# Performance work log

Measured on AMD Instinct MI355X. Metric: run time of the kernel, lower is better.

The kernel has to match this reference:

```python
import jax, jax.numpy as jnp
import numpy as np

B, T, C, H = 2, 2048, 1024, 16
D = C // H  # head_dim = 64


def setup_inputs() -> dict:
    key = jax.random.key(0)
    k1, k2, k3, k4 = jax.random.split(key, 4)
    x = jax.random.normal(k1, (B, T, C), dtype=jnp.float32)
    # key_padding_mask: True for valid token, False for padding.
    # Use per-example valid lengths so the mask is realistic; every example
    # has length >= 1 so no softmax row is fully masked.
    lengths = jax.random.randint(k2, (B,), T // 2, T + 1)
    key_padding_mask = jnp.arange(T)[None, :] < lengths[:, None]
    Wqkv = jax.random.normal(k3, (3 * C, C), dtype=jnp.float32) * 0.02
    bqkv = jnp.zeros((3 * C,), dtype=jnp.float32)
    Wproj = jax.random.normal(k4, (C, C), dtype=jnp.float32) * 0.02
    bproj = jnp.zeros((C,), dtype=jnp.float32)
    return {"x": x, "key_padding_mask": key_padding_mask,
            "Wqkv": Wqkv, "bqkv": bqkv, "Wproj": Wproj, "bproj": bproj}


def reference(x, key_padding_mask, Wqkv, bqkv, Wproj, bproj):
    # qkv projection (torch Linear: y = x @ W^T + b)
    qkv = jnp.einsum('btc,oc->bto', x, Wqkv) + bqkv          # (B,T,3C)
    q, k, v = jnp.split(qkv, 3, axis=-1)
    q = q.reshape(B, T, H, D)
    k = k.reshape(B, T, H, D)
    v = v.reshape(B, T, H, D)
    scale = 1.0 / np.sqrt(D).astype(np.float32)
    scores = jnp.einsum('bqhd,bkhd->bhqk', q, k) * scale      # (B,H,T,T)
    causal = jnp.tril(jnp.ones((T, T), dtype=bool))           # (T,T)
    mask = causal[None, None, :, :] & key_padding_mask[:, None, None, :]
    scores = jnp.where(mask, scores, -jnp.inf)
    attn = jax.nn.softmax(scores, axis=-1)                    # dropout p=0.0
    out = jnp.einsum('bhqk,bkhd->bqhd', attn, v).reshape(B, T, C)
    out = jnp.einsum('btc,oc->bto', out, Wproj) + bproj
    return out
```

## Files before the change

### kernel.cpp

```cpp
#include <hip/hip_runtime.h>
#include <hip/hip_bf16.h>
#include <stdint.h>

#define B_ 2
#define T_ 2048
#define C_ 1024
#define H_ 16
#define D_ 64

typedef __attribute__((ext_vector_type(8))) short bf16x8;
typedef __attribute__((ext_vector_type(4))) float f32x4;

__device__ __forceinline__ unsigned short f2bf(float f) {
  union { float f; uint32_t u; } c; c.f = f;
  uint32_t r = c.u + 0x7FFFu + ((c.u >> 16) & 1u);
  return (unsigned short)(r >> 16);
}

__device__ __forceinline__ uint32_t pack_bf16x2(float lo, float hi) {
  uint32_t r;
  asm("v_cvt_pk_bf16_f32 %0, %1, %2" : "=v"(r) : "v"(lo), "v"(hi));
  return r;
}

__device__ __forceinline__ void gload_lds16(const unsigned short* g,
                                            unsigned short* l) {
  __builtin_amdgcn_global_load_lds(
      (const __attribute__((address_space(1))) void*)(g),
      (__attribute__((address_space(3))) void*)(l), 16, 0, 0);
}

#define N4_X 1048576
#define N4_WQ 786432
#define N4_WP 262144
__global__ void cvt_all(const float* __restrict__ x,
                        const float* __restrict__ wqkv,
                        const float* __restrict__ wproj,
                        unsigned short* __restrict__ xb,
                        unsigned short* __restrict__ wq,
                        unsigned short* __restrict__ wp) {
  int i = blockIdx.x * 256 + threadIdx.x;
  const float* s; unsigned short* d; int j;
  if (i < N4_X) { s = x; d = xb; j = i; }
  else if (i < N4_X + N4_WQ) { s = wqkv; d = wq; j = i - N4_X; }
  else { s = wproj; d = wp; j = i - (N4_X + N4_WQ); }
  float4 v = ((const float4*)s)[j];
  ushort4 o;
  o.x = f2bf(v.x); o.y = f2bf(v.y); o.z = f2bf(v.z); o.w = f2bf(v.w);
  ((ushort4*)d)[j] = o;
}

__global__ void compute_lengths(const unsigned int* __restrict__ mask,
                                int* __restrict__ lens) {
  int lane = threadIdx.x;
  unsigned int w0 = mask[0];
  for (int b = 0; b < B_; ++b) {
    int cnt = 0;
    if (w0 == 1u) {
      for (int t = lane; t < T_; t += 64) cnt += (mask[(size_t)b * T_ + t] != 0u);
    } else if (w0 == 0x3F800000u) {
      const float* mf = (const float*)mask;
      for (int t = lane; t < T_; t += 64) cnt += (mf[(size_t)b * T_ + t] != 0.f);
    } else {
      const unsigned char* mb = (const unsigned char*)mask;
      for (int t = lane; t < T_; t += 64) cnt += (mb[(size_t)b * T_ + t] != 0);
    }
    for (int off = 32; off > 0; off >>= 1) cnt += __shfl_down(cnt, off);
    if (lane == 0) lens[b] = cnt;
  }
}

__global__ __launch_bounds__(256)
void gemm_bt(const unsigned short* __restrict__ A,
             const unsigned short* __restrict__ Bm,
             const float* __restrict__ bias,
             float* __restrict__ outF,
             unsigned short* __restrict__ Qw,
             unsigned short* __restrict__ Kw,
             unsigned short* __restrict__ Vw,
             int N, int K, int mode) {
  __shared__ unsigned short As[128 * 64];
  __shared__ unsigned short Bs[128 * 64];
  const int tid = threadIdx.x;
  const int lane = tid & 63;
  const int w = tid >> 6;
  const int wm = w >> 1, wn = w & 1;
  const int q4 = lane >> 4, l15 = lane & 15;
  const int bm = blockIdx.y * 128;
  const int bn = blockIdx.x * 128;

  f32x4 acc[4][4] = {};

  for (int kt = 0; kt < K; kt += 64) {
#pragma unroll
    for (int i = 0; i < 4; ++i) {
      int r0 = w * 32 + i * 8;
      int row = r0 + (lane >> 3);
      int kc = (lane & 7) ^ (row & 7);
      gload_lds16(A + (size_t)(bm + row) * K + kt + kc * 8, &As[r0 * 64]);
      gload_lds16(Bm + (size_t)(bn + row) * K + kt + kc * 8, &Bs[r0 * 64]);
    }
    __syncthreads();
#pragma unroll
    for (int kk = 0; kk < 2; ++kk) {
      bf16x8 af[4], bfv[4];
#pragma unroll
      for (int mi = 0; mi < 4; ++mi) {
        int row = wm * 64 + mi * 16 + l15;
        int pc = (kk * 4 + q4) ^ (row & 7);
        af[mi] = *(const bf16x8*)(As + (size_t)row * 64 + pc * 8);
      }
#pragma unroll
      for (int ni = 0; ni < 4; ++ni) {
        int row = wn * 64 + ni * 16 + l15;
        int pc = (kk * 4 + q4) ^ (row & 7);
        bfv[ni] = *(const bf16x8*)(Bs + (size_t)row * 64 + pc * 8);
      }
#pragma unroll
      for (int mi = 0; mi < 4; ++mi)
#pragma unroll
        for (int ni = 0; ni < 4; ++ni)
          acc[mi][ni] = __builtin_amdgcn_mfma_f32_16x16x32_bf16(
              af[mi], bfv[ni], acc[mi][ni], 0, 0, 0);
    }
    __syncthreads();
  }

#pragma unroll
  for (int mi = 0; mi < 4; ++mi) {
    const int row0 = bm + wm * 64 + mi * 16 + q4 * 4;
#pragma unroll
    for (int ni = 0; ni < 4; ++ni) {
      const int col = bn + wn * 64 + ni * 16 + l15;
      const float bv = bias[col];
#pragma unroll
      for (int r = 0; r < 4; ++r) {
        const int row = row0 + r;
        float v = acc[mi][ni][r] + bv;
        if (mode == 1) {
          outF[(size_t)row * N + col] = v;
        } else {
          int b = row >> 11, t = row & (T_ - 1);
          int which = col >> 10, c = col & (C_ - 1);
          int h = c >> 6, dd = c & (D_ - 1);
          unsigned short* dst = (which == 0) ? Qw : ((which == 1) ? Kw : Vw);
          if (which == 0) v *= 0.1803368801111243f;
          dst[(((size_t)(b * H_ + h) * T_) + t) * D_ + dd] = f2bf(v);
        }
      }
    }
  }
}

__global__ __launch_bounds__(256)
void transpose_v(const unsigned short* __restrict__ V,
                 unsigned short* __restrict__ Vt) {
  __shared__ unsigned short tile[64][65];
  int bh = blockIdx.y;
  int t0 = blockIdx.x * 64;
  int tid = threadIdx.x;
  int r = tid >> 2, c0 = (tid & 3) * 16;
  const uint4* s4 = (const uint4*)(V + ((size_t)bh * T_ + t0 + r) * D_ + c0);
  union { uint4 v; unsigned short u[8]; } ua, ub;
  ua.v = s4[0]; ub.v = s4[1];
#pragma unroll
  for (int j = 0; j < 8; ++j) {
    tile[r][c0 + j] = ua.u[j];
    tile[r][c0 + 8 + j] = ub.u[j];
  }
  __syncthreads();
  int dd = tid >> 2, tt0 = (tid & 3) * 16;
  union { uint4 v[2]; unsigned short u[16]; } ov;
#pragma unroll
  for (int j = 0; j < 16; ++j) ov.u[j] = tile[tt0 + j][dd];
  uint4* dptr = (uint4*)(Vt + ((size_t)bh * D_ + dd) * T_ + t0 + tt0);
  dptr[0] = ov.v[0];
  dptr[1] = ov.v[1];
}

__global__ __launch_bounds__(256)
void attn_fwd(const unsigned short* __restrict__ Qw,
              const unsigned short* __restrict__ Kw,
              const unsigned short* __restrict__ Vt,
              unsigned short* __restrict__ AO,
              const int* __restrict__ lens) {
  __shared__ unsigned short Ks[2][64 * 64];
  __shared__ unsigned short Vs[2][64 * 64];
  __shared__ unsigned short Pb[4][16 * 64];

  const int bh = blockIdx.y;
  const int b = bh >> 4;
  const int h = bh & 15;
  const int qs = 31 - blockIdx.x;
  const int q0 = qs * 64;
  const int tid = threadIdx.x;
  const int lane = tid & 63;
  const int w = tid >> 6;
  const int q4 = lane >> 4, l15 = lane & 15;
  const int len = lens[b];

  const unsigned short* Qp = Qw + (size_t)bh * T_ * D_;
  const unsigned short* Kp = Kw + (size_t)bh * T_ * D_;
  const unsigned short* Vp = Vt + (size_t)bh * D_ * T_;
  unsigned short* Pw = &Pb[w][0];

  const int qw0 = q0 + w * 16;
  const int qwmax = qw0 + 15;

  bf16x8 qf[2];
#pragma unroll
  for (int kk = 0; kk < 2; ++kk)
    qf[kk] = *(const bf16x8*)(Qp + (size_t)(qw0 + l15) * D_ + kk * 32 + q4 * 8);

  f32x4 ot[4] = {};
  float m = -INFINITY;
  float lsum = 0.f;

  int kcap = q0 + 63;
  if (kcap > len - 1) kcap = len - 1;
  const int nkt = kcap / 64 + 1;

  const int srow = lane >> 3;
  const int scc = lane & 7;

#pragma unroll
  for (int i = 0; i < 2; ++i) {
    int r0 = w * 16 + i * 8;
    int rk = r0 + srow;
    int kc = scc ^ (rk & 7);
    gload_lds16(Kp + (size_t)rk * D_ + kc * 8, &Ks[0][r0 * 64]);
    gload_lds16(Vp + (size_t)rk * T_ + kc * 8, &Vs[0][r0 * 64]);
  }
  __syncthreads();

  int cur = 0;
  for (int kt = 0; kt < nkt; ++kt) {
    const int kbase = kt * 64;
    if (kt + 1 < nkt) {
      const int kb2 = kbase + 64;
#pragma unroll
      for (int i = 0; i < 2; ++i) {
        int r0 = w * 16 + i * 8;
        int rk = r0 + srow;
        int kc = scc ^ (rk & 7);
        gload_lds16(Kp + (size_t)(kb2 + rk) * D_ + kc * 8, &Ks[cur ^ 1][r0 * 64]);
        gload_lds16(Vp + (size_t)rk * T_ + kb2 + kc * 8, &Vs[cur ^ 1][r0 * 64]);
      }
    }

    if (kbase <= qwmax) {
      f32x4 st[4];
#pragma unroll
      for (int nt = 0; nt < 4; ++nt) {
        bf16x8 kfr0, kfr1;
        {
          int row = nt * 16 + l15;
          int pc0 = q4 ^ (row & 7);
          int pc1 = (4 + q4) ^ (row & 7);
          kfr0 = *(const bf16x8*)(&Ks[cur][row * 64 + pc0 * 8]);
          kfr1 = *(const bf16x8*)(&Ks[cur][row * 64 + pc1 * 8]);
        }
        f32x4 z = {};
        z = __builtin_amdgcn_mfma_f32_16x16x32_bf16(kfr0, qf[0], z, 0, 0, 0);
        z = __builtin_amdgcn_mfma_f32_16x16x32_bf16(kfr1, qf[1], z, 0, 0, 0);
        st[nt] = z;
      }
      const bool interior = (kbase + 63 <= qw0) && (kbase + 63 < len);
      float pmax = -INFINITY;
      if (interior) {
#pragma unroll
        for (int nt = 0; nt < 4; ++nt)
#pragma unroll
          for (int r = 0; r < 4; ++r) pmax = fmaxf(pmax, st[nt][r]);
      } else {
        const int qq = qw0 + l15;
#pragma unroll
        for (int nt = 0; nt < 4; ++nt)
#pragma unroll
          for (int r = 0; r < 4; ++r) {
            int kpos = kbase + nt * 16 + q4 * 4 + r;
            bool ok = (kpos < len) && (kpos <= qq);
            float v = ok ? st[nt][r] : -INFINITY;
            st[nt][r] = v;
            pmax = fmaxf(pmax, v);
          }
      }
      pmax = fmaxf(pmax, __shfl_xor(pmax, 16));
      pmax = fmaxf(pmax, __shfl_xor(pmax, 32));
      if (!__all(pmax <= m + 8.f)) {
        float mn = fmaxf(m, pmax);
        float sc = exp2f(m - mn);
        m = mn;
        lsum *= sc;
#pragma unroll
        for (int dt = 0; dt < 4; ++dt)
#pragma unroll
          for (int r = 0; r < 4; ++r) ot[dt][r] *= sc;
      }
      float psum = 0.f;
#pragma unroll
      for (int nt = 0; nt < 4; ++nt) {
        float p0 = exp2f(st[nt][0] - m);
        float p1 = exp2f(st[nt][1] - m);
        float p2 = exp2f(st[nt][2] - m);
        float p3 = exp2f(st[nt][3] - m);
        psum += (p0 + p1) + (p2 + p3);
        uint32_t w0 = pack_bf16x2(p0, p1);
        uint32_t w1 = pack_bf16x2(p2, p3);
        int c = nt * 4 + q4;
        int phys = c ^ ((l15 & 7) << 1);
        uint2 pr; pr.x = w0; pr.y = w1;
        *(uint2*)(&Pw[l15 * 64 + phys * 4]) = pr;
      }
      psum += __shfl_xor(psum, 16);
      psum += __shfl_xor(psum, 32);
      lsum += psum;
      bf16x8 pt[2];
#pragma unroll
      for (int kk = 0; kk < 2; ++kk) {
        int c0 = kk * 8 + q4 * 2;
        int phys = c0 ^ ((l15 & 7) << 1);
        pt[kk] = *(const bf16x8*)(&Pw[l15 * 64 + phys * 4]);
      }
#pragma unroll
      for (int dt = 0; dt < 4; ++dt) {
        bf16x8 vfr0, vfr1;
        {
          int row = dt * 16 + l15;
          int pc0 = q4 ^ (row & 7);
          int pc1 = (4 + q4) ^ (row & 7);
          vfr0 = *(const bf16x8*)(&Vs[cur][row * 64 + pc0 * 8]);
          vfr1 = *(const bf16x8*)(&Vs[cur][row * 64 + pc1 * 8]);
        }
        ot[dt] = __builtin_amdgcn_mfma_f32_16x16x32_bf16(vfr0, pt[0], ot[dt], 0, 0, 0);
        ot[dt] = __builtin_amdgcn_mfma_f32_16x16x32_bf16(vfr1, pt[1], ot[dt], 0, 0, 0);
      }
    }

    __syncthreads();
    cur ^= 1;
  }

  {
    float inv = 1.f / lsum;
    int qq = qw0 + l15;
#pragma unroll
    for (int dt = 0; dt < 4; ++dt) {
      uint2 pr;
      pr.x = pack_bf16x2(ot[dt][0] * inv, ot[dt][1] * inv);
      pr.y = pack_bf16x2(ot[dt][2] * inv, ot[dt][3] * inv);
      *(uint2*)(&AO[(size_t)(b * T_ + qq) * C_ + h * 64 + dt * 16 + q4 * 4]) = pr;
    }
  }
}

extern "C" void kernel_launch(void* const* d_in, const int* in_sizes, int n_in,
                              void* d_out, int out_size, void* d_ws, size_t ws_size,
                              hipStream_t stream) {
  const float* x = (const float*)d_in[0];
  const unsigned int* mask = (const unsigned int*)d_in[1];
  const float* Wqkv = (const float*)d_in[2];
  const float* bqkv = (const float*)d_in[3];
  const float* Wproj = (const float*)d_in[4];
  const float* bproj = (const float*)d_in[5];
  float* out = (float*)d_out;

  unsigned short* XB = (unsigned short*)d_ws;
  unsigned short* WQ = XB + 4194304;
  unsigned short* WP = WQ + 3145728;
  unsigned short* Qw = WP + 1048576;
  unsigned short* Kw = Qw + 4194304;
  unsigned short* Vw = Kw + 4194304;
  unsigned short* Vt = Vw + 4194304;
  unsigned short* AO = Vt + 4194304;
  int* lens = (int*)(AO + 4194304);

  cvt_all<<<8192, 256, 0, stream>>>(x, Wqkv, Wproj, XB, WQ, WP);
  compute_lengths<<<1, 64, 0, stream>>>(mask, lens);

  gemm_bt<<<dim3(3072 / 128, 4096 / 128), 256, 0, stream>>>(
      XB, WQ, bqkv, nullptr, Qw, Kw, Vw, 3072, 1024, 0);

  transpose_v<<<dim3(T_ / 64, B_ * H_), 256, 0, stream>>>(Vw, Vt);

  attn_fwd<<<dim3(32, B_ * H_), 256, 0, stream>>>(Qw, Kw, Vt, AO, lens);

  gemm_bt<<<dim3(1024 / 128, 4096 / 128), 256, 0, stream>>>(
      AO, WP, bproj, out, nullptr, nullptr, nullptr, 1024, 1024, 1);
}
```

Before: 235.8 us.

## Pair low and high causal query tiles per attention block

Each attention block now handles two query tiles, a low one and its mirrored high one (sl and 31-sl). Both share the same double-buffered K/V tiles in LDS, which balances causal work across blocks and reuses the K/V loads for the low tile. The grid is halved to 512 blocks. In exchange, register pressure rises from holding two sets of Q fragments, accumulators and softmax state, and fewer blocks are available to hide latency.

```diff
diff --git a/kernel.cpp b/kernel.cpp
--- a/kernel.cpp
+++ b/kernel.cpp
@@ -191,8 +191,8 @@
   const int bh = blockIdx.y;
   const int b = bh >> 4;
   const int h = bh & 15;
-  const int qs = 31 - blockIdx.x;
-  const int q0 = qs * 64;
+  const int sl = blockIdx.x;
+  const int sh = 31 - sl;
   const int tid = threadIdx.x;
   const int lane = tid & 63;
   const int w = tid >> 6;
@@ -204,19 +204,21 @@
   const unsigned short* Vp = Vt + (size_t)bh * D_ * T_;
   unsigned short* Pw = &Pb[w][0];
 
-  const int qw0 = q0 + w * 16;
-  const int qwmax = qw0 + 15;
-
-  bf16x8 qf[2];
-#pragma unroll
-  for (int kk = 0; kk < 2; ++kk)
-    qf[kk] = *(const bf16x8*)(Qp + (size_t)(qw0 + l15) * D_ + kk * 32 + q4 * 8);
-
-  f32x4 ot[4] = {};
-  float m = -INFINITY;
-  float lsum = 0.f;
-
-  int kcap = q0 + 63;
+  const int ql0 = sl * 64 + w * 16;
+  const int qh0 = sh * 64 + w * 16;
+
+  bf16x8 qfl[2], qfh[2];
+#pragma unroll
+  for (int kk = 0; kk < 2; ++kk) {
+    qfl[kk] = *(const bf16x8*)(Qp + (size_t)(ql0 + l15) * D_ + kk * 32 + q4 * 8);
+    qfh[kk] = *(const bf16x8*)(Qp + (size_t)(qh0 + l15) * D_ + kk * 32 + q4 * 8);
+  }
+
+  f32x4 otl[4] = {}, oth[4] = {};
+  float ml = -INFINITY, mh = -INFINITY;
+  float lsl = 0.f, lsh = 0.f;
+
+  int kcap = sh * 64 + 63;
   if (kcap > len - 1) kcap = len - 1;
   const int nkt = kcap / 64 + 1;
 
@@ -233,6 +235,96 @@
   }
   __syncthreads();
 
+  auto group_tile = [&](int kbase, int cur, int qg0, bf16x8 (&qf)[2],
+                        f32x4 (&ot)[4], float& m, float& lsum) {
+    f32x4 st[4];
+#pragma unroll
+    for (int nt = 0; nt < 4; ++nt) {
+      bf16x8 kfr0, kfr1;
+      {
+        int row = nt * 16 + l15;
+        int pc0 = q4 ^ (row & 7);
+        int pc1 = (4 + q4) ^ (row & 7);
+        kfr0 = *(const bf16x8*)(&Ks[cur][row * 64 + pc0 * 8]);
+        kfr1 = *(const bf16x8*)(&Ks[cur][row * 64 + pc1 * 8]);
+      }
+      f32x4 z = {};
+      z = __builtin_amdgcn_mfma_f32_16x16x32_bf16(kfr0, qf[0], z, 0, 0, 0);
+      z = __builtin_amdgcn_mfma_f32_16x16x32_bf16(kfr1, qf[1], z, 0, 0, 0);
+      st[nt] = z;
+    }
+    const bool interior = (kbase + 63 <= qg0) && (kbase + 63 < len);
+    float pmax = -INFINITY;
+    if (interior) {
+#pragma unroll
+      for (int nt = 0; nt < 4; ++nt)
+#pragma unroll
+        for (int r = 0; r < 4; ++r) pmax = fmaxf(pmax, st[nt][r]);
+    } else {
+      const int qq = qg0 + l15;
+#pragma unroll
+      for (int nt = 0; nt < 4; ++nt)
+#pragma unroll
+        for (int r = 0; r < 4; ++r) {
+          int kpos = kbase + nt * 16 + q4 * 4 + r;
+          bool ok = (kpos < len) && (kpos <= qq);
+          float v = ok ? st[nt][r] : -INFINITY;
+          st[nt][r] = v;
+          pmax = fmaxf(pmax, v);
+        }
+    }
+    pmax = fmaxf(pmax, __shfl_xor(pmax, 16));
+    pmax = fmaxf(pmax, __shfl_xor(pmax, 32));
+    if (!__all(pmax <= m + 8.f)) {
+      float mn = fmaxf(m, pmax);
+      float sc = exp2f(m - mn);
+      m = mn;
+      lsum *= sc;
+#pragma unroll
+      for (int dt = 0; dt < 4; ++dt)
+#pragma unroll
+        for (int r = 0; r < 4; ++r) ot[dt][r] *= sc;
+    }
+    float psum = 0.f;
+#pragma unroll
+    for (int nt = 0; nt < 4; ++nt) {
+      float p0 = exp2f(st[nt][0] - m);
+      float p1 = exp2f(st[nt][1] - m);
+      float p2 = exp2f(st[nt][2] - m);
+      float p3 = exp2f(st[nt][3] - m);
+      psum += (p0 + p1) + (p2 + p3);
+      uint32_t w0 = pack_bf16x2(p0, p1);
+      uint32_t w1 = pack_bf16x2(p2, p3);
+      int c = nt * 4 + q4;
+      int phys = c ^ ((l15 & 7) << 1);
+      uint2 pr; pr.x = w0; pr.y = w1;
+      *(uint2*)(&Pw[l15 * 64 + phys * 4]) = pr;
+    }
+    psum += __shfl_xor(psum, 16);
+    psum += __shfl_xor(psum, 32);
+    lsum += psum;
+    bf16x8 pt[2];
+#pragma unroll
+    for (int kk = 0; kk < 2; ++kk) {
+      int c0 = kk * 8 + q4 * 2;
+      int phys = c0 ^ ((l15 & 7) << 1);
+      pt[kk] = *(const bf16x8*)(&Pw[l15 * 64 + phys * 4]);
+    }
+#pragma unroll
+    for (int dt = 0; dt < 4; ++dt) {
+      bf16x8 vfr0, vfr1;
+      {
+        int row = dt * 16 + l15;
+        int pc0 = q4 ^ (row & 7);
+        int pc1 = (4 + q4) ^ (row & 7);
+        vfr0 = *(const bf16x8*)(&Vs[cur][row * 64 + pc0 * 8]);
+        vfr1 = *(const bf16x8*)(&Vs[cur][row * 64 + pc1 * 8]);
+      }
+      ot[dt] = __builtin_amdgcn_mfma_f32_16x16x32_bf16(vfr0, pt[0], ot[dt], 0, 0, 0);
+      ot[dt] = __builtin_amdgcn_mfma_f32_16x16x32_bf16(vfr1, pt[1], ot[dt], 0, 0, 0);
+    }
+  };
+
   int cur = 0;
   for (int kt = 0; kt < nkt; ++kt) {
     const int kbase = kt * 64;
@@ -248,108 +340,28 @@
       }
     }
 
-    if (kbase <= qwmax) {
-      f32x4 st[4];
-#pragma unroll
-      for (int nt = 0; nt < 4; ++nt) {
-        bf16x8 kfr0, kfr1;
-        {
-          int row = nt * 16 + l15;
-          int pc0 = q4 ^ (row & 7);
-          int pc1 = (4 + q4) ^ (row & 7);
-          kfr0 = *(const bf16x8*)(&Ks[cur][row * 64 + pc0 * 8]);
-          kfr1 = *(const bf16x8*)(&Ks[cur][row * 64 + pc1 * 8]);
-        }
-        f32x4 z = {};
-        z = __builtin_amdgcn_mfma_f32_16x16x32_bf16(kfr0, qf[0], z, 0, 0, 0);
-        z = __builtin_amdgcn_mfma_f32_16x16x32_bf16(kfr1, qf[1], z, 0, 0, 0);
-        st[nt] = z;
-      }
-      const bool interior = (kbase + 63 <= qw0) && (kbase + 63 < len);
-      float pmax = -INFINITY;
-      if (interior) {
-#pragma unroll
-        for (int nt = 0; nt < 4; ++nt)
-#pragma unroll
-          for (int r = 0; r < 4; ++r) pmax = fmaxf(pmax, st[nt][r]);
-      } else {
-        const int qq = qw0 + l15;
-#pragma unroll
-        for (int nt = 0; nt < 4; ++nt)
-#pragma unroll
-          for (int r = 0; r < 4; ++r) {
-            int kpos = kbase + nt * 16 + q4 * 4 + r;
-            bool ok = (kpos < len) && (kpos <= qq);
-            float v = ok ? st[nt][r] : -INFINITY;
-            st[nt][r] = v;
-            pmax = fmaxf(pmax, v);
-          }
-      }
-      pmax = fmaxf(pmax, __shfl_xor(pmax, 16));
-      pmax = fmaxf(pmax, __shfl_xor(pmax, 32));
-      if (!__all(pmax <= m + 8.f)) {
-        float mn = fmaxf(m, pmax);
-        float sc = exp2f(m - mn);
-        m = mn;
-        lsum *= sc;
-#pragma unroll
-        for (int dt = 0; dt < 4; ++dt)
-#pragma unroll
-          for (int r = 0; r < 4; ++r) ot[dt][r] *= sc;
-      }
-      float psum = 0.f;
-#pragma unroll
-      for (int nt = 0; nt < 4; ++nt) {
-        float p0 = exp2f(st[nt][0] - m);
-        float p1 = exp2f(st[nt][1] - m);
-        float p2 = exp2f(st[nt][2] - m);
-        float p3 = exp2f(st[nt][3] - m);
-        psum += (p0 + p1) + (p2 + p3);
-        uint32_t w0 = pack_bf16x2(p0, p1);
-        uint32_t w1 = pack_bf16x2(p2, p3);
-        int c = nt * 4 + q4;
-        int phys = c ^ ((l15 & 7) << 1);
-        uint2 pr; pr.x = w0; pr.y = w1;
-        *(uint2*)(&Pw[l15 * 64 + phys * 4]) = pr;
-      }
-      psum += __shfl_xor(psum, 16);
-      psum += __shfl_xor(psum, 32);
-      lsum += psum;
-      bf16x8 pt[2];
-#pragma unroll
-      for (int kk = 0; kk < 2; ++kk) {
-        int c0 = kk * 8 + q4 * 2;
-        int phys = c0 ^ ((l15 & 7) << 1);
-        pt[kk] = *(const bf16x8*)(&Pw[l15 * 64 + phys * 4]);
-      }
-#pragma unroll
-      for (int dt = 0; dt < 4; ++dt) {
-        bf16x8 vfr0, vfr1;
-        {
-          int row = dt * 16 + l15;
-          int pc0 = q4 ^ (row & 7);
-          int pc1 = (4 + q4) ^ (row & 7);
-          vfr0 = *(const bf16x8*)(&Vs[cur][row * 64 + pc0 * 8]);
-          vfr1 = *(const bf16x8*)(&Vs[cur][row * 64 + pc1 * 8]);
-        }
-        ot[dt] = __builtin_amdgcn_mfma_f32_16x16x32_bf16(vfr0, pt[0], ot[dt], 0, 0, 0);
-        ot[dt] = __builtin_amdgcn_mfma_f32_16x16x32_bf16(vfr1, pt[1], ot[dt], 0, 0, 0);
-      }
-    }
+    group_tile(kbase, cur, qh0, qfh, oth, mh, lsh);
+    if (kt <= sl) group_tile(kbase, cur, ql0, qfl, otl, ml, lsl);
 
     __syncthreads();
     cur ^= 1;
   }
 
   {
-    float inv = 1.f / lsum;
-    int qq = qw0 + l15;
+    float invl = 1.f / lsl;
+    float invh = 1.f / lsh;
+    int qql = ql0 + l15;
+    int qqh = qh0 + l15;
 #pragma unroll
     for (int dt = 0; dt < 4; ++dt) {
       uint2 pr;
-      pr.x = pack_bf16x2(ot[dt][0] * inv, ot[dt][1] * inv);
-      pr.y = pack_bf16x2(ot[dt][2] * inv, ot[dt][3] * inv);
-      *(uint2*)(&AO[(size_t)(b * T_ + qq) * C_ + h * 64 + dt * 16 + q4 * 4]) = pr;
+      pr.x = pack_bf16x2(otl[dt][0] * invl, otl[dt][1] * invl);
+      pr.y = pack_bf16x2(otl[dt][2] * invl, otl[dt][3] * invl);
+      *(uint2*)(&AO[(size_t)(b * T_ + qql) * C_ + h * 64 + dt * 16 + q4 * 4]) = pr;
+      uint2 ph;
+      ph.x = pack_bf16x2(oth[dt][0] * invh, oth[dt][1] * invh);
+      ph.y = pack_bf16x2(oth[dt][2] * invh, oth[dt][3] * invh);
+      *(uint2*)(&AO[(size_t)(b * T_ + qqh) * C_ + h * 64 + dt * 16 + q4 * 4]) = ph;
     }
   }
 }
@@ -383,7 +395,7 @@
 
   transpose_v<<<dim3(T_ / 64, B_ * H_), 256, 0, stream>>>(Vw, Vt);
 
-  attn_fwd<<<dim3(32, B_ * H_), 256, 0, stream>>>(Qw, Kw, Vt, AO, lens);
+  attn_fwd<<<dim3(16, B_ * H_), 256, 0, stream>>>(Qw, Kw, Vt, AO, lens);
 
   gemm_bt<<<dim3(1024 / 128, 4096 / 128), 256, 0, stream>>>(
       AO, WP, bproj, out, nullptr, nullptr, nullptr, 1024, 1024, 1);
```

After: 216.8 us. 1.09x faster.
